# Kernel optimization log

Hardware: AMD Instinct MI355X
Metric: run time of the kernel (lower is better)

Reference implementation:

```python
import jax, jax.numpy as jnp
import numpy as np

HASH = 1 << 12
EPS = 1e-5
_OFFS = [(dx, dy, dz) for dx in (-1, 0, 1) for dy in (-1, 0, 1) for dz in (-1, 0, 1)]
_KOFF = [k for k, o in enumerate(_OFFS) if o != (0, 0, 0)]  # 26 non-center taps
_CENTER = 13


def _hkey(c):
    c = c.astype(np.int64)
    return (c[:, 0] * HASH + c[:, 1]) * HASH + c[:, 2]


def _rand_coords(rng, n, R):
    idx = rng.choice(R ** 3, size=n, replace=False)
    return np.stack(np.unravel_index(idx, (R, R, R)), axis=1).astype(np.int64)


def _conv3_maps(coords):
    # ME kernel map for a 3x3x3 stride-1 conv (in coords == out coords):
    # per non-center tap, (gather_idx, scatter_idx) pairs found by hash lookup.
    n = coords.shape[0]
    keys = _hkey(coords)
    order = np.argsort(keys)
    skeys = keys[order]
    ins, outs = [], []
    for k in _KOFF:
        qk = _hkey(coords + np.asarray(_OFFS[k], np.int64))
        pos = np.clip(np.searchsorted(skeys, qk), 0, n - 1)
        valid = skeys[pos] == qk
        outs.append(np.nonzero(valid)[0].astype(np.int32))
        ins.append(order[pos[valid]].astype(np.int32))
    m = max(len(a) for a in ins)
    im = np.zeros((26, m), np.int32)    # pad gathers with row 0
    om = np.full((26, m), n, np.int32)  # pad scatters into scrap row n (dropped)
    for j in range(26):
        im[j, :len(ins[j])] = ins[j]
        om[j, :len(outs[j])] = outs[j]
    return np.stack([im, om])  # [2, 26, M]


def _children(coords):
    # generative transpose conv k=2 s=2 output coords, ordered o*n + i
    offs = np.array([[a, b, c] for a in (0, 1) for b in (0, 1) for c in (0, 1)], np.int64)
    return (2 * coords[None] + offs[:, None]).reshape(-1, 3)


def _union(ca, cb):
    # sparse-tensor addition domain: union of coordinate sets
    ka, kb = _hkey(ca), _hkey(cb)
    ku = np.unique(np.concatenate([ka, kb]))
    cu = np.stack([ku // (HASH * HASH), (ku // HASH) % HASH, ku % HASH], axis=1)
    return cu, np.searchsorted(ku, ka).astype(np.int32), np.searchsorted(ku, kb).astype(np.int32)


def _sconv3(x, W, m):
    # sparse 3^3 conv as gather-GEMM-scatter; center tap is a plain GEMM
    n = x.shape[0]
    acc = jnp.zeros((n + 1, W.shape[2]), x.dtype)
    for j, k in enumerate(_KOFF):
        acc = acc.at[m[1, j]].add(x[m[0, j]] @ W[k])
    return acc[:n] + x @ W[_CENTER]


def _bn_elu(x, p):
    # MinkowskiBatchNorm (training-mode batch stats over active voxels) + ELU
    mu = jnp.mean(x, axis=0)
    var = jnp.mean(jnp.square(x - mu), axis=0)
    return jax.nn.elu(p[0] * (x - mu) * jax.lax.rsqrt(var + EPS) + p[1])


def _up_block(x, Wt, Wc, m, pa, pb):
    # generative transpose conv (every voxel emits 8 children, order o*n+i) -> BN -> ELU -> conv3 -> BN -> ELU
    t = jnp.einsum('nc,ocd->ond', x, Wt).reshape(-1, Wt.shape[2])
    return _bn_elu(_sconv3(_bn_elu(t, pa), Wc, m), pb)


def setup_inputs() -> dict:
    rng = np.random.default_rng(0)
    N2, N1, N0 = 1200, 6000, 16000
    C2 = _rand_coords(rng, N2, 40)
    C1 = _rand_coords(rng, N1, 80)
    C0 = _rand_coords(rng, N0, 160)
    G2 = _children(C2)                       # coords after up_block_2 transpose conv
    U1, lat1_idx, up1_idx = _union(C1, G2)   # inputs[1] + x domain
    G1 = _children(U1)
    U0, lat0_idx, up0_idx = _union(C0, G1)   # inputs[0] + x domain

    key = jax.random.key(0)
    ks = list(jax.random.split(key, 32))
    kit = iter(ks)

    def w(shape, fan_in):
        return jax.random.normal(next(kit), shape, jnp.float32) * np.float32(1.0 / np.sqrt(fan_in))

    def bn(c):
        g = 1.0 + 0.1 * jax.random.normal(next(kit), (c,), jnp.float32)
        b = 0.1 * jax.random.normal(next(kit), (c,), jnp.float32)
        return jnp.stack([g, b])

    return dict(
        feats0=jax.random.normal(next(kit), (N0, 64), jnp.float32),
        feats1=jax.random.normal(next(kit), (N1, 128), jnp.float32),
        feats2=jax.random.normal(next(kit), (N2, 256), jnp.float32),
        w_out0=w((27, 64, 128), 27 * 64),
        w_out1=w((27, 128, 128), 27 * 128),
        w_out2=w((27, 256, 128), 27 * 256),
        wt2=w((8, 256, 128), 256),
        wu2=w((27, 128, 128), 27 * 128),
        wt1=w((8, 128, 64), 128),
        wu1=w((27, 64, 64), 27 * 64),
        bn_out0=bn(128), bn_out1=bn(128), bn_out2=bn(128),
        bn_up2a=bn(128), bn_up2b=bn(128),
        bn_up1a=bn(64), bn_up1b=bn(64),
        u1_base=jnp.zeros((U1.shape[0], 128), jnp.float32),
        u0_base=jnp.zeros((U0.shape[0], 64), jnp.float32),
        m_c2=jnp.asarray(_conv3_maps(C2)),
        m_g2=jnp.asarray(_conv3_maps(G2)),
        m_u1=jnp.asarray(_conv3_maps(U1)),
        m_g1=jnp.asarray(_conv3_maps(G1)),
        m_u0=jnp.asarray(_conv3_maps(U0)),
        lat1_idx=jnp.asarray(lat1_idx), up1_idx=jnp.asarray(up1_idx),
        lat0_idx=jnp.asarray(lat0_idx), up0_idx=jnp.asarray(up0_idx),
    )


def reference(feats0, feats1, feats2, w_out0, w_out1, w_out2, wt2, wu2, wt1, wu1,
              bn_out0, bn_out1, bn_out2, bn_up2a, bn_up2b, bn_up1a, bn_up1b,
              u1_base, u0_base, m_c2, m_g2, m_u1, m_g1, m_u0,
              lat1_idx, up1_idx, lat0_idx, up0_idx):
    # i = 2 (top)
    out2 = _bn_elu(_sconv3(feats2, w_out2, m_c2), bn_out2)
    t = _up_block(feats2, wt2, wu2, m_g2, bn_up2a, bn_up2b)
    # i = 1: sparse add over union of coords, then out/up blocks
    x1 = u1_base.at[lat1_idx].add(feats1).at[up1_idx].add(t)
    out1 = _bn_elu(_sconv3(x1, w_out1, m_u1), bn_out1)
    t = _up_block(x1, wt1, wu1, m_g1, bn_up1a, bn_up1b)
    # i = 0
    x0 = u0_base.at[lat0_idx].add(feats0).at[up0_idx].add(t)
    out0 = _bn_elu(_sconv3(x0, w_out0, m_u0), bn_out0)
    return out0, out1, out2
```

## Files before the change

### kernel.cpp

```cpp
#include <hip/hip_runtime.h>

typedef __bf16 bf16x8 __attribute__((ext_vector_type(8)));
typedef float  f32x4  __attribute__((ext_vector_type(4)));

__device__ __forceinline__ float b2f(unsigned short u) {
    union { unsigned int i; float f; } v; v.i = ((unsigned int)u) << 16; return v.f;
}
__device__ __forceinline__ unsigned short f2b(float f) {
    union { float f; unsigned int i; } v; v.f = f;
    unsigned int u = v.i;
    return (unsigned short)((u + 0x7fffu + ((u >> 16) & 1u)) >> 16);
}

__global__ void table_init(int* __restrict__ tab, int n)
{
    int idx = blockIdx.x * blockDim.x + threadIdx.x;
    if (idx >= n * 27) return;
    tab[idx] = ((idx % 27) == 13) ? (idx / 27) : n;
}

__global__ void table_fill(int* __restrict__ tab, const int* __restrict__ map, int M, int n)
{
    int tid = blockIdx.x * blockDim.x + threadIdx.x;
    if (tid >= 26 * M) return;
    int j = tid / M, q = tid - j * M;
    int om = map[(26 + j) * M + q];
    if (om < n) {
        int k = (j < 13) ? j : j + 1;
        tab[om * 27 + k] = map[j * M + q];
    }
}

__global__ void pack_w(const float* __restrict__ W, unsigned short* __restrict__ P,
                       int total, int log2Cout, int log2KC)
{
    int tid = blockIdx.x * blockDim.x + threadIdx.x;
    if (tid >= total) return;
    int jj   = tid & 7;
    int cout = (tid >> 3) & ((1 << log2Cout) - 1);
    int rest = tid >> (3 + log2Cout);
    int quad = rest & 3;
    int kj   = rest >> 2;
    int kc   = kj & ((1 << log2KC) - 1);
    int j    = kj >> log2KC;
    int Cin  = (1 << log2KC) * 32;
    int Cout = 1 << log2Cout;
    P[tid] = f2b(W[((size_t)j * Cin + kc * 32 + quad * 8 + jj) * Cout + cout]);
}

__global__ void cast_bf16(const float* __restrict__ X, unsigned short* __restrict__ Y, int nElem)
{
    int tid = blockIdx.x * blockDim.x + threadIdx.x;
    if (tid < nElem) Y[tid] = f2b(X[tid]);
}

template<int T, int KC, int RT, bool OUTBF16>
__global__ __launch_bounds__(256) void conv_mfma_st(
    const unsigned short* __restrict__ Xb, const unsigned short* __restrict__ P,
    const int* __restrict__ tab, void* __restrict__ OutV, float* __restrict__ St,
    int n, int nblk)
{
    constexpr int Cin = KC * 32, Cout = 64 * T;
    constexpr int ROWS = RT * 16;
    constexpr int STRIDE = KC * 32 + 8;
    constexpr int CHUNKS = KC * 4;
    constexpr int RPR = 256 / CHUNKS;
    constexpr int NRD = ROWS / RPR;
    __shared__ int tps[ROWS * 27];
    __shared__ unsigned short abuf[2][ROWS * STRIDE];

    const int t = threadIdx.x, lane = t & 63, wv = t >> 6;
    const int m = lane & 15, quad = lane >> 4;

    const int q = nblk >> 3, rr = nblk & 7;
    const int xcd = blockIdx.x & 7, pos = blockIdx.x >> 3;
    const int bswz = (xcd < rr) ? (xcd * (q + 1) + pos) : (rr * (q + 1) + (xcd - rr) * q + pos);
    const int r0 = bswz * ROWS;
    int rows = n - r0; if (rows > ROWS) rows = ROWS;

    for (int e = t; e < ROWS * 27; e += 256)
        tps[e] = (e < rows * 27) ? tab[(size_t)r0 * 27 + e] : n;
    __syncthreads();

    const int sr = t / CHUNKS, sc = t % CHUNKS;

    f32x4 acc[RT][T];
    #pragma unroll
    for (int rt = 0; rt < RT; rt++)
        #pragma unroll
        for (int c = 0; c < T; c++) acc[rt][c] = f32x4{0.f, 0.f, 0.f, 0.f};

    uint4 sreg[NRD];

    #pragma unroll
    for (int rd = 0; rd < NRD; rd++) {
        int in = tps[(rd * RPR + sr) * 27 + 0];
        sreg[rd] = *reinterpret_cast<const uint4*>(Xb + (size_t)in * Cin + sc * 8);
    }
    #pragma unroll
    for (int rd = 0; rd < NRD; rd++)
        *reinterpret_cast<uint4*>(&abuf[0][(rd * RPR + sr) * STRIDE + sc * 8]) = sreg[rd];
    #pragma unroll
    for (int rd = 0; rd < NRD; rd++) {
        int in = tps[(rd * RPR + sr) * 27 + 1];
        sreg[rd] = *reinterpret_cast<const uint4*>(Xb + (size_t)in * Cin + sc * 8);
    }
    __syncthreads();

    for (int j = 0; j < 27; j++) {
        const int cur = j & 1;
        #pragma unroll
        for (int kc = 0; kc < KC; kc++) {
            bf16x8 a[RT];
            #pragma unroll
            for (int rt = 0; rt < RT; rt++)
                a[rt] = *reinterpret_cast<const bf16x8*>(&abuf[cur][(rt * 16 + m) * STRIDE + kc * 32 + quad * 8]);
            const unsigned short* bp = P + ((size_t)((j * KC + kc) * 4 + quad) * Cout + wv * (T * 16)) * 8;
            #pragma unroll
            for (int c = 0; c < T; c++) {
                bf16x8 b = *reinterpret_cast<const bf16x8*>(bp + (c * 16 + m) * 8);
                #pragma unroll
                for (int rt = 0; rt < RT; rt++)
                    acc[rt][c] = __builtin_amdgcn_mfma_f32_16x16x32_bf16(a[rt], b, acc[rt][c], 0, 0, 0);
            }
        }
        if (j + 1 < 27) {
            #pragma unroll
            for (int rd = 0; rd < NRD; rd++)
                *reinterpret_cast<uint4*>(&abuf[cur ^ 1][(rd * RPR + sr) * STRIDE + sc * 8]) = sreg[rd];
            if (j + 2 < 27) {
                #pragma unroll
                for (int rd = 0; rd < NRD; rd++) {
                    int in = tps[(rd * RPR + sr) * 27 + j + 2];
                    sreg[rd] = *reinterpret_cast<const uint4*>(Xb + (size_t)in * Cin + sc * 8);
                }
            }
        }
        __syncthreads();
    }

    #pragma unroll
    for (int c = 0; c < T; c++) {
        const int cout = (wv * T + c) * 16 + m;
        float s = 0.f, ss = 0.f;
        #pragma unroll
        for (int rt = 0; rt < RT; rt++) {
            #pragma unroll
            for (int reg = 0; reg < 4; reg++) {
                int r = rt * 16 + quad * 4 + reg;
                if (r < rows) {
                    float v = acc[rt][c][reg];
                    size_t off = (size_t)(r0 + r) * Cout + cout;
                    if (OUTBF16) {
                        unsigned short h = f2b(v);
                        ((unsigned short*)OutV)[off] = h;
                        v = b2f(h);
                    } else {
                        ((float*)OutV)[off] = v;
                    }
                    s += v; ss += v * v;
                }
            }
        }
        if (St) {
            s  += __shfl_xor(s, 16);  ss += __shfl_xor(ss, 16);
            s  += __shfl_xor(s, 32);  ss += __shfl_xor(ss, 32);
            if (quad == 0) {
                atomicAdd(&St[cout], s);
                atomicAdd(&St[Cout + cout], ss);
            }
        }
    }
}

template<int T, int RB, bool OUTBF16>
__global__ __launch_bounds__(256) void conv_mfma(
    const unsigned short* __restrict__ Xb, const unsigned short* __restrict__ P,
    const int* __restrict__ tab, void* __restrict__ OutV, int n, int Cin, int KC, int nblk)
{
    const int Cout = 64 * T;
    const int ROWS = RB * 16;
    __shared__ int tps[RB * 16 * 27];
    __shared__ int vld[27];
    const int t = threadIdx.x, lane = t & 63, wv = t >> 6;
    const int m = lane & 15, quad = lane >> 4;

    const int q = nblk >> 3, rr = nblk & 7;
    const int xcd = blockIdx.x & 7, pos = blockIdx.x >> 3;
    const int bswz = (xcd < rr) ? (xcd * (q + 1) + pos) : (rr * (q + 1) + (xcd - rr) * q + pos);
    const int r0 = bswz * ROWS;
    int rows = n - r0; if (rows > ROWS) rows = ROWS;

    for (int e = t; e < ROWS * 27; e += 256)
        tps[e] = (e < rows * 27) ? tab[(size_t)r0 * 27 + e] : n;
    __syncthreads();
    if constexpr (RB == 1) {
        if (t < 27) {
            int v = 0;
            for (int r = 0; r < 16; r++) v |= (tps[r * 27 + t] < n) ? 1 : 0;
            vld[t] = v;
        }
        __syncthreads();
    }

    f32x4 acc[RB][T];
    #pragma unroll
    for (int rt = 0; rt < RB; rt++)
        #pragma unroll
        for (int c = 0; c < T; c++) acc[rt][c] = f32x4{0.f, 0.f, 0.f, 0.f};

    const unsigned short* Xq = Xb + quad * 8;
    const unsigned short* Pq = P + ((size_t)quad * Cout + wv * (T * 16)) * 8;

    for (int j = 0; j < 27; j++) {
        if constexpr (RB == 1) {
            if (!vld[j]) continue;
        }
        int in[RB];
        #pragma unroll
        for (int rt = 0; rt < RB; rt++) in[rt] = tps[(rt * 16 + m) * 27 + j];
        for (int kc = 0; kc < KC; kc++) {
            bf16x8 a[RB];
            #pragma unroll
            for (int rt = 0; rt < RB; rt++)
                a[rt] = *reinterpret_cast<const bf16x8*>(Xq + (size_t)in[rt] * Cin + kc * 32);
            const unsigned short* bp = Pq + (size_t)((j * KC + kc) * 4) * Cout * 8;
            #pragma unroll
            for (int c = 0; c < T; c++) {
                bf16x8 b = *reinterpret_cast<const bf16x8*>(bp + (c * 16 + m) * 8);
                #pragma unroll
                for (int rt = 0; rt < RB; rt++)
                    acc[rt][c] = __builtin_amdgcn_mfma_f32_16x16x32_bf16(a[rt], b, acc[rt][c], 0, 0, 0);
            }
        }
    }

    #pragma unroll
    for (int c = 0; c < T; c++) {
        int cout = (wv * T + c) * 16 + m;
        #pragma unroll
        for (int rt = 0; rt < RB; rt++) {
            #pragma unroll
            for (int reg = 0; reg < 4; reg++) {
                int r = rt * 16 + quad * 4 + reg;
                if (r < rows) {
                    size_t off = (size_t)(r0 + r) * Cout + cout;
                    if (OUTBF16) ((unsigned short*)OutV)[off] = f2b(acc[rt][c][reg]);
                    else         ((float*)OutV)[off] = acc[rt][c][reg];
                }
            }
        }
    }
}

template<int KC, int T>
__global__ __launch_bounds__(256) void tconv_mfma(
    const unsigned short* __restrict__ Xb, const unsigned short* __restrict__ P,
    unsigned short* __restrict__ Out, int n)
{
    const int Cin = KC * 32, Cout = 64 * T;
    const int t = threadIdx.x, lane = t & 63, wv = t >> 6;
    const int m = lane & 15, quad = lane >> 4;
    const int r0 = blockIdx.x * 16;
    int rows = n - r0; if (rows > 16) rows = 16;

    bf16x8 a[KC];
    #pragma unroll
    for (int kc = 0; kc < KC; kc++) {
        a[kc] = bf16x8{};
        if (m < rows)
            a[kc] = *reinterpret_cast<const bf16x8*>(Xb + (size_t)(r0 + m) * Cin + kc * 32 + quad * 8);
    }

    for (int o = 0; o < 8; o++) {
        f32x4 acc[T];
        #pragma unroll
        for (int c = 0; c < T; c++) acc[c] = f32x4{0.f, 0.f, 0.f, 0.f};
        #pragma unroll
        for (int kc = 0; kc < KC; kc++) {
            const unsigned short* bp = P + ((size_t)((o * KC + kc) * 4 + quad) * Cout + wv * (T * 16)) * 8;
            #pragma unroll
            for (int c = 0; c < T; c++) {
                bf16x8 b = *reinterpret_cast<const bf16x8*>(bp + (c * 16 + m) * 8);
                acc[c] = __builtin_amdgcn_mfma_f32_16x16x32_bf16(a[kc], b, acc[c], 0, 0, 0);
            }
        }
        #pragma unroll
        for (int c = 0; c < T; c++) {
            int cout = (wv * T + c) * 16 + m;
            #pragma unroll
            for (int reg = 0; reg < 4; reg++) {
                int r = quad * 4 + reg;
                if (r < rows)
                    Out[((size_t)o * n + r0 + r) * Cout + cout] = f2b(acc[c][reg]);
            }
        }
    }
}

__global__ void scatter_add_f32(float* __restrict__ dst, const float* __restrict__ src,
                                const int* __restrict__ idx, long total, int C)
{
    long tid = (long)blockIdx.x * blockDim.x + threadIdx.x;
    if (tid >= total) return;
    long r = tid / C;
    int  c = (int)(tid - r * C);
    dst[(long)idx[r] * C + c] += src[tid];
}

__global__ void scatter_add_b16(float* __restrict__ dst, const unsigned short* __restrict__ src,
                                const int* __restrict__ idx, long total, int C)
{
    long tid = (long)blockIdx.x * blockDim.x + threadIdx.x;
    if (tid >= total) return;
    long r = tid / C;
    int  c = (int)(tid - r * C);
    dst[(long)idx[r] * C + c] += b2f(src[tid]);
}

template<bool BF16>
__global__ void bn_stats_k(const void* __restrict__ Xv, float* __restrict__ stats,
                           int n, int C, int rowsPerBlock)
{
    const int t = threadIdx.x;
    const int c = t & (C - 1);
    const int sub = t / C;
    const int nsub = 256 / C;
    int r0 = blockIdx.x * rowsPerBlock + sub;
    int r1 = blockIdx.x * rowsPerBlock + rowsPerBlock;
    if (r1 > n) r1 = n;
    float s = 0.f, ss = 0.f;
    for (int r = r0; r < r1; r += nsub) {
        float v = BF16 ? b2f(((const unsigned short*)Xv)[(long)r * C + c])
                       : ((const float*)Xv)[(long)r * C + c];
        s += v; ss += v * v;
    }
    __shared__ float bs[256];
    __shared__ float bq[256];
    bs[t] = s; bq[t] = ss;
    __syncthreads();
    if (sub == 0) {
        for (int k = 1; k < nsub; k++) { s += bs[k * C + c]; ss += bq[k * C + c]; }
        atomicAdd(&stats[c], s);
        atomicAdd(&stats[C + c], ss);
    }
}

template<bool BF16>
__global__ void bn_apply_k(void* __restrict__ Xv, const float* __restrict__ stats,
                           const float* __restrict__ gb, long total, int C, float invn)
{
    long tid = (long)blockIdx.x * blockDim.x + threadIdx.x;
    if (tid >= total) return;
    int c = (int)(tid & (C - 1));
    float mu  = stats[c] * invn;
    float var = stats[C + c] * invn - mu * mu;
    float sc  = gb[c] * rsqrtf(var + 1e-5f);
    float x   = BF16 ? b2f(((unsigned short*)Xv)[tid]) : ((float*)Xv)[tid];
    float v   = (x - mu) * sc + gb[C + c];
    v = (v > 0.f) ? v : expm1f(v);
    if (BF16) ((unsigned short*)Xv)[tid] = f2b(v);
    else      ((float*)Xv)[tid] = v;
}

extern "C" void kernel_launch(void* const* d_in, const int* in_sizes, int n_in,
                              void* d_out, int out_size, void* d_ws, size_t ws_size,
                              hipStream_t stream)
{
    const float* feats0  = (const float*)d_in[0];
    const float* feats1  = (const float*)d_in[1];
    const float* feats2  = (const float*)d_in[2];
    const float* w_out0  = (const float*)d_in[3];
    const float* w_out1  = (const float*)d_in[4];
    const float* w_out2  = (const float*)d_in[5];
    const float* wt2     = (const float*)d_in[6];
    const float* wu2     = (const float*)d_in[7];
    const float* wt1     = (const float*)d_in[8];
    const float* wu1     = (const float*)d_in[9];
    const float* bn_out0 = (const float*)d_in[10];
    const float* bn_out1 = (const float*)d_in[11];
    const float* bn_out2 = (const float*)d_in[12];
    const float* bn_up2a = (const float*)d_in[13];
    const float* bn_up2b = (const float*)d_in[14];
    const float* bn_up1a = (const float*)d_in[15];
    const float* bn_up1b = (const float*)d_in[16];
    const int* m_c2 = (const int*)d_in[19];
    const int* m_g2 = (const int*)d_in[20];
    const int* m_u1 = (const int*)d_in[21];
    const int* m_g1 = (const int*)d_in[22];
    const int* m_u0 = (const int*)d_in[23];
    const int* lat1 = (const int*)d_in[24];
    const int* up1  = (const int*)d_in[25];
    const int* lat0 = (const int*)d_in[26];
    const int* up0  = (const int*)d_in[27];

    const int N0  = in_sizes[0] / 64;
    const int N1  = in_sizes[1] / 128;
    const int N2  = in_sizes[2] / 256;
    const int U1  = in_sizes[17] / 128;
    const int U0  = in_sizes[18] / 64;
    const int G2n = in_sizes[25];
    const int G1n = in_sizes[27];
    const int Mc2 = in_sizes[19] / 52;
    const int Mg2 = in_sizes[20] / 52;
    const int Mu1 = in_sizes[21] / 52;
    const int Mg1 = in_sizes[22] / 52;
    const int Mu0 = in_sizes[23] / 52;

    float* out0 = (float*)d_out;
    float* out1 = out0 + (size_t)U0 * 128;
    float* out2 = out1 + (size_t)U1 * 128;

    char* wp = (char*)d_ws;
    auto alloc = [&](size_t bytes) -> char* {
        char* r = wp; wp += (bytes + 255) & ~(size_t)255; return r;
    };
    float*          x0   = (float*)alloc((size_t)U0 * 64 * 4);
    unsigned short* t1   = (unsigned short*)alloc((size_t)(G1n + 1) * 64 * 2);
    unsigned short* t1c  = (unsigned short*)alloc((size_t)(G1n + 1) * 64 * 2);
    unsigned short* t2   = (unsigned short*)alloc((size_t)(G2n + 1) * 128 * 2);
    unsigned short* t2c  = (unsigned short*)alloc((size_t)(G2n + 1) * 128 * 2);
    float*          x1   = (float*)alloc((size_t)U1 * 128 * 4);
    unsigned short* x1b  = (unsigned short*)alloc((size_t)(U1 + 1) * 128 * 2);
    unsigned short* x0b  = (unsigned short*)alloc((size_t)(U0 + 1) * 64 * 2);
    unsigned short* f2bb = (unsigned short*)alloc((size_t)(N2 + 1) * 256 * 2);
    unsigned short* pc2  = (unsigned short*)alloc((size_t)27 * 256 * 128 * 2);
    unsigned short* pt2  = (unsigned short*)alloc((size_t)8  * 256 * 128 * 2);
    unsigned short* pg2  = (unsigned short*)alloc((size_t)27 * 128 * 128 * 2);
    unsigned short* pu1  = (unsigned short*)alloc((size_t)27 * 128 * 128 * 2);
    unsigned short* pt1  = (unsigned short*)alloc((size_t)8  * 128 * 64  * 2);
    unsigned short* pg1  = (unsigned short*)alloc((size_t)27 * 64  * 64  * 2);
    unsigned short* pu0  = (unsigned short*)alloc((size_t)27 * 64  * 128 * 2);
    int maxSmall = (U1 > G2n) ? U1 : G2n;
    int*   smallTab = (int*)alloc((size_t)maxSmall * 27 * 4);
    float* stats    = (float*)alloc(1024);
    int* tab_g1 = (int*)x0;
    int* tab_u0 = (int*)t1;

    hipMemsetAsync(f2bb + (size_t)N2  * 256, 0, 256 * 2, stream);
    hipMemsetAsync(t2   + (size_t)G2n * 128, 0, 128 * 2, stream);
    hipMemsetAsync(x1b  + (size_t)U1  * 128, 0, 128 * 2, stream);
    hipMemsetAsync(t1   + (size_t)G1n * 64,  0, 64  * 2, stream);
    hipMemsetAsync(x0b  + (size_t)U0  * 64,  0, 64  * 2, stream);

    auto packW = [&](const float* W, unsigned short* P, int taps, int l2co, int l2kc) {
        int total = taps * ((1 << l2kc) * 32) * (1 << l2co);
        pack_w<<<dim3((total + 255) / 256), dim3(256), 0, stream>>>(W, P, total, l2co, l2kc);
    };
    auto cast = [&](const float* X, unsigned short* Y, long nElem) {
        cast_bf16<<<dim3((int)((nElem + 255) / 256)), dim3(256), 0, stream>>>(X, Y, (int)nElem);
    };
    auto buildTab = [&](int* tab, const int* map, int M, int n) {
        table_init<<<dim3((n * 27 + 255) / 256), dim3(256), 0, stream>>>(tab, n);
        table_fill<<<dim3((26 * M + 255) / 256), dim3(256), 0, stream>>>(tab, map, M, n);
    };
    auto conv = [&](const unsigned short* Xb, const unsigned short* P, const int* tab,
                    void* Out, int n, int Cin, int Cout, bool outbf16, float* st) {
        int KC = Cin / 32;
        if (n >= 40000 && KC == 2) {
            int nblk = (n + 127) / 128;
            dim3 g(nblk), b(256);
            if (Cout == 128) {
                if (outbf16) conv_mfma_st<2, 2, 8, true ><<<g, b, 0, stream>>>(Xb, P, tab, Out, st, n, nblk);
                else         conv_mfma_st<2, 2, 8, false><<<g, b, 0, stream>>>(Xb, P, tab, Out, st, n, nblk);
            } else {
                if (outbf16) conv_mfma_st<1, 2, 8, true ><<<g, b, 0, stream>>>(Xb, P, tab, Out, st, n, nblk);
                else         conv_mfma_st<1, 2, 8, false><<<g, b, 0, stream>>>(Xb, P, tab, Out, st, n, nblk);
            }
            return;
        }
        if (n >= 12000) {
            int nblk = (n + 63) / 64;
            dim3 g(nblk), b(256);
            if (Cout == 128 && KC == 4) {
                if (outbf16) conv_mfma_st<2, 4, 4, true ><<<g, b, 0, stream>>>(Xb, P, tab, Out, st, n, nblk);
                else         conv_mfma_st<2, 4, 4, false><<<g, b, 0, stream>>>(Xb, P, tab, Out, st, n, nblk);
                return;
            }
            if (Cout == 128 && KC == 2) {
                if (outbf16) conv_mfma_st<2, 2, 4, true ><<<g, b, 0, stream>>>(Xb, P, tab, Out, st, n, nblk);
                else         conv_mfma_st<2, 2, 4, false><<<g, b, 0, stream>>>(Xb, P, tab, Out, st, n, nblk);
                return;
            }
            if (Cout == 64 && KC == 2) {
                if (outbf16) conv_mfma_st<1, 2, 4, true ><<<g, b, 0, stream>>>(Xb, P, tab, Out, st, n, nblk);
                else         conv_mfma_st<1, 2, 4, false><<<g, b, 0, stream>>>(Xb, P, tab, Out, st, n, nblk);
                return;
            }
        }
        int RB = (n >= 12000) ? 2 : 1;
        int nblk = (n + RB * 16 - 1) / (RB * 16);
        dim3 g(nblk), b(256);
        #define CONV_CASE(T_, RB_)                                                                        \
            if (Cout == 64 * T_ && RB == RB_) {                                                           \
                if (outbf16) conv_mfma<T_, RB_, true ><<<g, b, 0, stream>>>(Xb, P, tab, Out, n, Cin, KC, nblk); \
                else         conv_mfma<T_, RB_, false><<<g, b, 0, stream>>>(Xb, P, tab, Out, n, Cin, KC, nblk); \
                return;                                                                                   \
            }
        CONV_CASE(2, 2) CONV_CASE(2, 1)
        CONV_CASE(1, 2) CONV_CASE(1, 1)
        #undef CONV_CASE
    };
    auto bnapply = [&](void* X, const float* gb, int n, int C, bool bf16) {
        long total = (long)n * C;
        if (bf16) bn_apply_k<true ><<<dim3((int)((total + 255) / 256)), dim3(256), 0, stream>>>(X, stats, gb, total, C, 1.0f / n);
        else      bn_apply_k<false><<<dim3((int)((total + 255) / 256)), dim3(256), 0, stream>>>(X, stats, gb, total, C, 1.0f / n);
    };
    auto bnelu = [&](void* X, const float* gb, int n, int C, bool bf16) {
        hipMemsetAsync(stats, 0, 2 * C * sizeof(float), stream);
        const int rpb = 512;
        if (bf16) bn_stats_k<true ><<<dim3((n + rpb - 1) / rpb), dim3(256), 0, stream>>>(X, stats, n, C, rpb);
        else      bn_stats_k<false><<<dim3((n + rpb - 1) / rpb), dim3(256), 0, stream>>>(X, stats, n, C, rpb);
        bnapply(X, gb, n, C, bf16);
    };

    cast(feats2, f2bb, (long)N2 * 256);
    packW(w_out2, pc2, 27, 7, 3);
    packW(wt2,    pt2,  8, 7, 3);
    packW(wu2,    pg2, 27, 7, 2);
    packW(w_out1, pu1, 27, 7, 2);
    packW(wt1,    pt1,  8, 6, 2);
    packW(wu1,    pg1, 27, 6, 1);
    packW(w_out0, pu0, 27, 7, 1);

    buildTab(smallTab, m_c2, Mc2, N2);
    conv(f2bb, pc2, smallTab, out2, N2, 256, 128, false, nullptr);
    bnelu(out2, bn_out2, N2, 128, false);
    tconv_mfma<8, 2><<<dim3((N2 + 15) / 16), dim3(256), 0, stream>>>(f2bb, pt2, t2, N2);
    bnelu(t2, bn_up2a, G2n, 128, true);
    buildTab(smallTab, m_g2, Mg2, G2n);
    conv(t2, pg2, smallTab, t2c, G2n, 128, 128, true, nullptr);
    bnelu(t2c, bn_up2b, G2n, 128, true);

    hipMemsetAsync(x1, 0, (size_t)U1 * 128 * sizeof(float), stream);
    {
        long tot = (long)N1 * 128;
        scatter_add_f32<<<dim3((int)((tot + 255) / 256)), dim3(256), 0, stream>>>(x1, feats1, lat1, tot, 128);
        tot = (long)G2n * 128;
        scatter_add_b16<<<dim3((int)((tot + 255) / 256)), dim3(256), 0, stream>>>(x1, t2c, up1, tot, 128);
    }
    cast(x1, x1b, (long)U1 * 128);
    buildTab(smallTab, m_u1, Mu1, U1);
    hipMemsetAsync(stats, 0, 2 * 128 * sizeof(float), stream);
    conv(x1b, pu1, smallTab, out1, U1, 128, 128, false, stats);
    bnapply(out1, bn_out1, U1, 128, false);
    tconv_mfma<4, 1><<<dim3((U1 + 15) / 16), dim3(256), 0, stream>>>(x1b, pt1, t1, U1);
    bnelu(t1, bn_up1a, G1n, 64, true);
    buildTab(tab_g1, m_g1, Mg1, G1n);
    hipMemsetAsync(stats, 0, 2 * 64 * sizeof(float), stream);
    conv(t1, pg1, tab_g1, t1c, G1n, 64, 64, true, stats);
    bnapply(t1c, bn_up1b, G1n, 64, true);

    hipMemsetAsync(x0, 0, (size_t)U0 * 64 * sizeof(float), stream);
    {
        long tot = (long)N0 * 64;
        scatter_add_f32<<<dim3((int)((tot + 255) / 256)), dim3(256), 0, stream>>>(x0, feats0, lat0, tot, 64);
        tot = (long)G1n * 64;
        scatter_add_b16<<<dim3((int)((tot + 255) / 256)), dim3(256), 0, stream>>>(x0, t1c, up0, tot, 64);
    }
    buildTab(tab_u0, m_u0, Mu0, U0);
    cast(x0, x0b, (long)U0 * 64);
    hipMemsetAsync(stats, 0, 2 * 128 * sizeof(float), stream);
    conv(x0b, pu0, tab_u0, out0, U0, 64, 128, false, stats);
    bnapply(out0, bn_out0, U0, 128, false);
}
```

Before: 1.114 ms.

## Prefetch gathers before MFMA, replicate BN stat atomics per XCD, retune conv tiles

The gather-conv main loop now writes the next A tile to LDS and issues the global gather for tap j+2 before the MFMA work on tap j. This uses two register staging sets so the load latency overlaps compute, at the cost of more VGPRs. The BN-statistic atomics are spread across 8 copies indexed by blockIdx&7, and bn_apply sums the copies, which cuts contention on the atomics. Conv launch configs also change: the 128-row path for large n is removed and the KC=4 case uses 32-row blocks.

```diff
diff --git a/kernel.cpp b/kernel.cpp
--- a/kernel.cpp
+++ b/kernel.cpp
@@ -82,7 +82,8 @@
         tps[e] = (e < rows * 27) ? tab[(size_t)r0 * 27 + e] : n;
     __syncthreads();
 
-    const int sr = t / CHUNKS, sc = t % CHUNKS;
+    const int sr = t / CHUNKS;
+    const int sc = t % CHUNKS;
 
     f32x4 acc[RT][T];
     #pragma unroll
@@ -90,25 +91,37 @@
         #pragma unroll
         for (int c = 0; c < T; c++) acc[rt][c] = f32x4{0.f, 0.f, 0.f, 0.f};
 
-    uint4 sreg[NRD];
+    uint4 sreg[2][NRD];
 
     #pragma unroll
     for (int rd = 0; rd < NRD; rd++) {
         int in = tps[(rd * RPR + sr) * 27 + 0];
-        sreg[rd] = *reinterpret_cast<const uint4*>(Xb + (size_t)in * Cin + sc * 8);
+        sreg[0][rd] = *reinterpret_cast<const uint4*>(Xb + (size_t)in * Cin + sc * 8);
     }
     #pragma unroll
     for (int rd = 0; rd < NRD; rd++)
-        *reinterpret_cast<uint4*>(&abuf[0][(rd * RPR + sr) * STRIDE + sc * 8]) = sreg[rd];
+        *reinterpret_cast<uint4*>(&abuf[0][(rd * RPR + sr) * STRIDE + sc * 8]) = sreg[0][rd];
     #pragma unroll
     for (int rd = 0; rd < NRD; rd++) {
         int in = tps[(rd * RPR + sr) * 27 + 1];
-        sreg[rd] = *reinterpret_cast<const uint4*>(Xb + (size_t)in * Cin + sc * 8);
+        sreg[1][rd] = *reinterpret_cast<const uint4*>(Xb + (size_t)in * Cin + sc * 8);
     }
     __syncthreads();
 
     for (int j = 0; j < 27; j++) {
         const int cur = j & 1;
+        if (j + 1 < 27) {
+            #pragma unroll
+            for (int rd = 0; rd < NRD; rd++)
+                *reinterpret_cast<uint4*>(&abuf[cur ^ 1][(rd * RPR + sr) * STRIDE + sc * 8]) = sreg[(j + 1) & 1][rd];
+        }
+        if (j + 2 < 27) {
+            #pragma unroll
+            for (int rd = 0; rd < NRD; rd++) {
+                int in = tps[(rd * RPR + sr) * 27 + j + 2];
+                sreg[j & 1][rd] = *reinterpret_cast<const uint4*>(Xb + (size_t)in * Cin + sc * 8);
+            }
+        }
         #pragma unroll
         for (int kc = 0; kc < KC; kc++) {
             bf16x8 a[RT];
@@ -122,18 +135,6 @@
                 #pragma unroll
                 for (int rt = 0; rt < RT; rt++)
                     acc[rt][c] = __builtin_amdgcn_mfma_f32_16x16x32_bf16(a[rt], b, acc[rt][c], 0, 0, 0);
-            }
-        }
-        if (j + 1 < 27) {
-            #pragma unroll
-            for (int rd = 0; rd < NRD; rd++)
-                *reinterpret_cast<uint4*>(&abuf[cur ^ 1][(rd * RPR + sr) * STRIDE + sc * 8]) = sreg[rd];
-            if (j + 2 < 27) {
-                #pragma unroll
-                for (int rd = 0; rd < NRD; rd++) {
-                    int in = tps[(rd * RPR + sr) * 27 + j + 2];
-                    sreg[rd] = *reinterpret_cast<const uint4*>(Xb + (size_t)in * Cin + sc * 8);
-                }
             }
         }
         __syncthreads();
@@ -166,8 +167,9 @@
             s  += __shfl_xor(s, 16);  ss += __shfl_xor(ss, 16);
             s  += __shfl_xor(s, 32);  ss += __shfl_xor(ss, 32);
             if (quad == 0) {
-                atomicAdd(&St[cout], s);
-                atomicAdd(&St[Cout + cout], ss);
+                float* Sr = St + (size_t)(blockIdx.x & 7) * 2 * Cout;
+                atomicAdd(&Sr[cout], s);
+                atomicAdd(&Sr[Cout + cout], ss);
             }
         }
     }
@@ -348,13 +350,18 @@
 
 template<bool BF16>
 __global__ void bn_apply_k(void* __restrict__ Xv, const float* __restrict__ stats,
-                           const float* __restrict__ gb, long total, int C, float invn)
+                           const float* __restrict__ gb, long total, int C, float invn, int nrep)
 {
     long tid = (long)blockIdx.x * blockDim.x + threadIdx.x;
     if (tid >= total) return;
     int c = (int)(tid & (C - 1));
-    float mu  = stats[c] * invn;
-    float var = stats[C + c] * invn - mu * mu;
+    float sm = 0.f, sq = 0.f;
+    for (int r = 0; r < nrep; r++) {
+        sm += stats[r * 2 * C + c];
+        sq += stats[r * 2 * C + C + c];
+    }
+    float mu  = sm * invn;
+    float var = sq * invn - mu * mu;
     float sc  = gb[c] * rsqrtf(var + 1e-5f);
     float x   = BF16 ? b2f(((unsigned short*)Xv)[tid]) : ((float*)Xv)[tid];
     float v   = (x - mu) * sc + gb[C + c];
@@ -433,7 +440,7 @@
     unsigned short* pu0  = (unsigned short*)alloc((size_t)27 * 64  * 128 * 2);
     int maxSmall = (U1 > G2n) ? U1 : G2n;
     int*   smallTab = (int*)alloc((size_t)maxSmall * 27 * 4);
-    float* stats    = (float*)alloc(1024);
+    float* stats    = (float*)alloc(8 * 2 * 128 * 4);
     int* tab_g1 = (int*)x0;
     int* tab_u0 = (int*)t1;
 
@@ -457,34 +464,26 @@
     auto conv = [&](const unsigned short* Xb, const unsigned short* P, const int* tab,
                     void* Out, int n, int Cin, int Cout, bool outbf16, float* st) {
         int KC = Cin / 32;
-        if (n >= 40000 && KC == 2) {
-            int nblk = (n + 127) / 128;
-            dim3 g(nblk), b(256);
-            if (Cout == 128) {
-                if (outbf16) conv_mfma_st<2, 2, 8, true ><<<g, b, 0, stream>>>(Xb, P, tab, Out, st, n, nblk);
-                else         conv_mfma_st<2, 2, 8, false><<<g, b, 0, stream>>>(Xb, P, tab, Out, st, n, nblk);
-            } else {
-                if (outbf16) conv_mfma_st<1, 2, 8, true ><<<g, b, 0, stream>>>(Xb, P, tab, Out, st, n, nblk);
-                else         conv_mfma_st<1, 2, 8, false><<<g, b, 0, stream>>>(Xb, P, tab, Out, st, n, nblk);
-            }
-            return;
-        }
         if (n >= 12000) {
-            int nblk = (n + 63) / 64;
-            dim3 g(nblk), b(256);
-            if (Cout == 128 && KC == 4) {
-                if (outbf16) conv_mfma_st<2, 4, 4, true ><<<g, b, 0, stream>>>(Xb, P, tab, Out, st, n, nblk);
-                else         conv_mfma_st<2, 4, 4, false><<<g, b, 0, stream>>>(Xb, P, tab, Out, st, n, nblk);
-                return;
-            }
             if (Cout == 128 && KC == 2) {
+                int nblk = (n + 63) / 64;
+                dim3 g(nblk), b(256);
                 if (outbf16) conv_mfma_st<2, 2, 4, true ><<<g, b, 0, stream>>>(Xb, P, tab, Out, st, n, nblk);
                 else         conv_mfma_st<2, 2, 4, false><<<g, b, 0, stream>>>(Xb, P, tab, Out, st, n, nblk);
                 return;
             }
             if (Cout == 64 && KC == 2) {
+                int nblk = (n + 63) / 64;
+                dim3 g(nblk), b(256);
                 if (outbf16) conv_mfma_st<1, 2, 4, true ><<<g, b, 0, stream>>>(Xb, P, tab, Out, st, n, nblk);
                 else         conv_mfma_st<1, 2, 4, false><<<g, b, 0, stream>>>(Xb, P, tab, Out, st, n, nblk);
+                return;
+            }
+            if (Cout == 128 && KC == 4) {
+                int nblk = (n + 31) / 32;
+                dim3 g(nblk), b(256);
+                if (outbf16) conv_mfma_st<2, 4, 2, true ><<<g, b, 0, stream>>>(Xb, P, tab, Out, st, n, nblk);
+                else         conv_mfma_st<2, 4, 2, false><<<g, b, 0, stream>>>(Xb, P, tab, Out, st, n, nblk);
                 return;
             }
         }
@@ -501,17 +500,17 @@
         CONV_CASE(1, 2) CONV_CASE(1, 1)
         #undef CONV_CASE
     };
-    auto bnapply = [&](void* X, const float* gb, int n, int C, bool bf16) {
+    auto bnapply = [&](void* X, const float* gb, int n, int C, bool bf16, int nrep) {
         long total = (long)n * C;
-        if (bf16) bn_apply_k<true ><<<dim3((int)((total + 255) / 256)), dim3(256), 0, stream>>>(X, stats, gb, total, C, 1.0f / n);
-        else      bn_apply_k<false><<<dim3((int)((total + 255) / 256)), dim3(256), 0, stream>>>(X, stats, gb, total, C, 1.0f / n);
+        if (bf16) bn_apply_k<true ><<<dim3((int)((total + 255) / 256)), dim3(256), 0, stream>>>(X, stats, gb, total, C, 1.0f / n, nrep);
+        else      bn_apply_k<false><<<dim3((int)((total + 255) / 256)), dim3(256), 0, stream>>>(X, stats, gb, total, C, 1.0f / n, nrep);
     };
     auto bnelu = [&](void* X, const float* gb, int n, int C, bool bf16) {
         hipMemsetAsync(stats, 0, 2 * C * sizeof(float), stream);
         const int rpb = 512;
         if (bf16) bn_stats_k<true ><<<dim3((n + rpb - 1) / rpb), dim3(256), 0, stream>>>(X, stats, n, C, rpb);
         else      bn_stats_k<false><<<dim3((n + rpb - 1) / rpb), dim3(256), 0, stream>>>(X, stats, n, C, rpb);
-        bnapply(X, gb, n, C, bf16);
+        bnapply(X, gb, n, C, bf16, 1);
     };
 
     cast(feats2, f2bb, (long)N2 * 256);
@@ -541,15 +540,15 @@
     }
     cast(x1, x1b, (long)U1 * 128);
     buildTab(smallTab, m_u1, Mu1, U1);
-    hipMemsetAsync(stats, 0, 2 * 128 * sizeof(float), stream);
+    hipMemsetAsync(stats, 0, 8 * 2 * 128 * sizeof(float), stream);
     conv(x1b, pu1, smallTab, out1, U1, 128, 128, false, stats);
-    bnapply(out1, bn_out1, U1, 128, false);
+    bnapply(out1, bn_out1, U1, 128, false, 8);
     tconv_mfma<4, 1><<<dim3((U1 + 15) / 16), dim3(256), 0, stream>>>(x1b, pt1, t1, U1);
     bnelu(t1, bn_up1a, G1n, 64, true);
     buildTab(tab_g1, m_g1, Mg1, G1n);
-    hipMemsetAsync(stats, 0, 2 * 64 * sizeof(float), stream);
+    hipMemsetAsync(stats, 0, 8 * 2 * 64 * sizeof(float), stream);
     conv(t1, pg1, tab_g1, t1c, G1n, 64, 64, true, stats);
-    bnapply(t1c, bn_up1b, G1n, 64, true);
+    bnapply(t1c, bn_up1b, G1n, 64, true, 8);
 
     hipMemsetAsync(x0, 0, (size_t)U0 * 64 * sizeof(float), stream);
     {
@@ -560,7 +559,7 @@
     }
     buildTab(tab_u0, m_u0, Mu0, U0);
     cast(x0, x0b, (long)U0 * 64);
-    hipMemsetAsync(stats, 0, 2 * 128 * sizeof(float), stream);
+    hipMemsetAsync(stats, 0, 8 * 2 * 128 * sizeof(float), stream);
     conv(x0b, pu0, tab_u0, out0, U0, 64, 128, false, stats);
-    bnapply(out0, bn_out0, U0, 128, false);
-}
+    bnapply(out0, bn_out0, U0, 128, false, 8);
+}
```

After: 1.220 ms. 9.5% more time.
